# Optimization experiments

Hardware: AMD Instinct MI355X
Metric: run time of the kernel (lower is better)

## Reference

```python
import jax, jax.numpy as jnp
import numpy as np

BS, T, G, C = 64, 128, 36, 256
H = 256          # gaze LSTM hidden
P = 256          # spatial projected size
PT = 256         # temporal projected size
Q = 16           # queue size
NC = 10          # num classes
NEG = -1e9


def setup_inputs() -> dict:
    key = jax.random.key(0)
    ks = jax.random.split(key, 40)
    s = 0.02
    D = C + H
    inp = {
        'cnn_feat_seq': jax.random.normal(ks[0], (BS, T, G, C), jnp.float32),
        'gaze_seq': jax.random.normal(ks[1], (BS, T, 3), jnp.float32),
        # init-hidden / init-cell MLPs (Linear(3,H), Tanh, Linear(H,H), Tanh)
        'init_h_w1': jax.random.normal(ks[2], (H, 3)) * s, 'init_h_b1': jnp.zeros((H,)),
        'init_h_w2': jax.random.normal(ks[3], (H, H)) * s, 'init_h_b2': jnp.zeros((H,)),
        'init_c_w1': jax.random.normal(ks[4], (H, 3)) * s, 'init_c_b1': jnp.zeros((H,)),
        'init_c_w2': jax.random.normal(ks[5], (H, H)) * s, 'init_c_b2': jnp.zeros((H,)),
        # LSTM (input 3, hidden H), torch gate order i,f,g,o
        'lstm_wih': jax.random.normal(ks[6], (4 * H, 3)) * s, 'lstm_whh': jax.random.normal(ks[7], (4 * H, H)) * s,
        'lstm_bih': jnp.zeros((4 * H,)), 'lstm_bhh': jnp.zeros((4 * H,)),
        # spatial attention
        'sa_wl': jax.random.normal(ks[8], (P, H)) * s, 'sa_bl': jnp.zeros((P,)),
        'sa_wc': jax.random.normal(ks[9], (P, C)) * s, 'sa_bc': jnp.zeros((P,)),
        'sa_wz': jax.random.normal(ks[10], (P,)) * s,
        # temporal attention
        'ta_wl': jax.random.normal(ks[11], (PT, H)) * s, 'ta_bl': jnp.zeros((PT,)),
        'ta_wv': jax.random.normal(ks[12], (PT, C)) * s, 'ta_bv': jnp.zeros((PT,)),
        'ta_wz': jax.random.normal(ks[13], (PT,)) * s,
        # MLP classifier: Linear(D,D) -> Linear(D,D) -> Linear(D,NC), no nonlinearity
        'mlp_w1': jax.random.normal(ks[14], (D, D)) * s, 'mlp_b1': jnp.zeros((D,)),
        'mlp_w2': jax.random.normal(ks[15], (D, D)) * s, 'mlp_b2': jnp.zeros((D,)),
        'mlp_w3': jax.random.normal(ks[16], (NC, D)) * s, 'mlp_b3': jnp.zeros((NC,)),
    }
    return inp


def _forward(cnn_feat_seq, gaze_seq,
             init_h_w1, init_h_b1, init_h_w2, init_h_b2,
             init_c_w1, init_c_b1, init_c_w2, init_c_b2,
             lstm_wih, lstm_whh, lstm_bih, lstm_bhh,
             sa_wl, sa_bl, sa_wc, sa_bc, sa_wz,
             ta_wl, ta_bl, ta_wv, ta_bv, ta_wz,
             mlp_w1, mlp_b1, mlp_w2, mlp_b2, mlp_w3, mlp_b3):
    bs, num_frame = gaze_seq.shape[0], gaze_seq.shape[1]
    mean_gaze = jnp.mean(gaze_seq, axis=1)  # (bs, 3)
    # init MLP ends with Tanh, and forward applies F.tanh again
    h0 = jnp.tanh(jnp.tanh(jnp.tanh(mean_gaze @ init_h_w1.T + init_h_b1) @ init_h_w2.T + init_h_b2))
    c0 = jnp.tanh(jnp.tanh(jnp.tanh(mean_gaze @ init_c_w1.T + init_c_b1) @ init_c_w2.T + init_c_b2))
    buf_s0 = jnp.zeros((Q, bs, C), cnn_feat_seq.dtype)
    buf_h0 = jnp.zeros((Q, bs, H), cnn_feat_seq.dtype)
    qidx = jnp.arange(Q)

    def step(carry, xs):
        h, c, buf_s, buf_h, i = carry
        feat, gaze = xs  # (bs,G,C), (bs,3)
        # --- spatial additive attention over grids ---
        Hp = h @ sa_wl.T + sa_bl                                  # (bs,P)
        Vp = jnp.einsum('bgc,pc->bgp', feat, sa_wc) + sa_bc       # (bs,G,P)
        zs = jnp.tanh(Hp[:, None, :] + Vp) @ sa_wz                # (bs,G)
        sw = jax.nn.softmax(zs, axis=1)
        spat = jnp.einsum('bgc,bg->bc', feat, sw)                 # (bs,C)
        # --- rolling queues (newest last) ---
        buf_s = jnp.concatenate([buf_s[1:], spat[None]], axis=0)
        buf_h = jnp.concatenate([buf_h[1:], h[None]], axis=0)
        count = jnp.minimum(i + 1, Q)
        mask = qidx >= (Q - count)                                # (Q,) valid slots
        # --- temporal additive attention over queue ---
        Hq = jnp.einsum('qbh,ph->qbp', buf_h, ta_wl) + ta_bl
        Vq = jnp.einsum('qbc,pc->qbp', buf_s, ta_wv) + ta_bv
        zt = jnp.tanh(Hq + Vq) @ ta_wz                            # (Q,bs)
        zt = jnp.where(mask[:, None], zt, NEG)
        tw = jax.nn.softmax(zt, axis=0)
        temp = jnp.einsum('qbc,qb->bc', buf_s, tw)                # (bs,C)
        # --- one LSTM step on gaze ---
        gates = gaze @ lstm_wih.T + lstm_bih + h @ lstm_whh.T + lstm_bhh
        gi, gf, gg, go = jnp.split(gates, 4, axis=-1)
        c = jax.nn.sigmoid(gf) * c + jax.nn.sigmoid(gi) * jnp.tanh(gg)
        h = jax.nn.sigmoid(go) * jnp.tanh(c)
        # --- classifier on concat(temporal_feat, lstm_hidden) ---
        fc = jnp.concatenate([temp, h], axis=1)                   # (bs, C+H)
        pred = ((fc @ mlp_w1.T + mlp_b1) @ mlp_w2.T + mlp_b2) @ mlp_w3.T + mlp_b3
        return (h, c, buf_s, buf_h, i + 1), pred

    feats_t = jnp.swapaxes(cnn_feat_seq, 0, 1)  # (T,bs,G,C)
    gaze_t = jnp.swapaxes(gaze_seq, 0, 1)       # (T,bs,3)
    _, preds = jax.lax.scan(step, (h0, c0, buf_s0, buf_h0, jnp.int32(0)), (feats_t, gaze_t))
    # torch cats (1,bs,NC) pieces along dim=1 -> (1, T*bs, NC)
    return preds.reshape(1, num_frame * bs, NC)


def reference(cnn_feat_seq, gaze_seq,
              init_h_w1, init_h_b1, init_h_w2, init_h_b2,
              init_c_w1, init_c_b1, init_c_w2, init_c_b2,
              lstm_wih, lstm_whh, lstm_bih, lstm_bhh,
              sa_wl, sa_bl, sa_wc, sa_bc, sa_wz,
              ta_wl, ta_bl, ta_wv, ta_bv, ta_wz,
              mlp_w1, mlp_b1, mlp_w2, mlp_b2, mlp_w3, mlp_b3):
    return _forward(cnn_feat_seq, gaze_seq,
                    init_h_w1, init_h_b1, init_h_w2, init_h_b2,
                    init_c_w1, init_c_b1, init_c_w2, init_c_b2,
                    lstm_wih, lstm_whh, lstm_bih, lstm_bhh,
                    sa_wl, sa_bl, sa_wc, sa_bc, sa_wz,
                    ta_wl, ta_bl, ta_wv, ta_bv, ta_wz,
                    mlp_w1, mlp_b1, mlp_w2, mlp_b2, mlp_w3, mlp_b3)
```

## Files before the change

### kernel.cpp

```cpp
#include <hip/hip_runtime.h>
#include <cstdint>
#include <cstddef>

#define BSZ 64
#define TT  128
#define GG  36
#define CC  256
#define HH  256
#define QQ  16
#define NCLS 10
#define NROW 8192

using short8  = __attribute__((ext_vector_type(8))) short;
using f32x4   = __attribute__((ext_vector_type(4))) float;
using half2_t = __attribute__((ext_vector_type(2))) _Float16;
typedef unsigned int u32;
typedef unsigned short u16;

#define OFF_WI    0u
#define OFF_WF    131072u
#define OFF_WG    262144u
#define OFF_WO    393216u
#define OFF_SAWL  524288u
#define OFF_TAWL  655360u
#define OFF_TAWV  786432u
#define OFF_SAWC  917504u
#define OFF_W32   1048576u
#define OFF_WC    1069056u
#define OFF_BC    1089536u
#define OFF_H0F16 1089792u
#define OFF_C0    1122560u
#define OFF_HSEQ  1188096u
#define OFF_HSEQB 9642240u
#define OFF_HPSA  13869312u
#define OFF_HQ    22257920u
#define OFF_SPAT  30646528u
#define OFF_SPATB 39035136u
#define OFF_ZSC   43229440u
#define WS_NEEDED 43262208u

__device__ __forceinline__ float fast_sig(float x){ return 1.f/(1.f+__expf(-x)); }
__device__ __forceinline__ float fast_tanh(float x){ float e=__expf(2.f*x); return 1.f-2.f/(e+1.f); }
__device__ __forceinline__ u16 f2bf(float f){
  u32 u = __builtin_bit_cast(u32, f);
  u += 0x7fffu + ((u>>16)&1u);
  return (u16)(u>>16);
}
__device__ __forceinline__ float bf2f(u16 b){
  u32 u = ((u32)b)<<16; return __builtin_bit_cast(float, u);
}
__device__ __forceinline__ u32 packf16(float a, float b){
  half2_t h; h.x = (_Float16)a; h.y = (_Float16)b;
  return __builtin_bit_cast(u32, h);
}
__device__ __forceinline__ float dot2(u32 w, u32 h, float acc){
#if __has_builtin(__builtin_amdgcn_fdot2)
  return __builtin_amdgcn_fdot2(__builtin_bit_cast(half2_t, w),
                                __builtin_bit_cast(half2_t, h), acc, false);
#else
  half2_t a = __builtin_bit_cast(half2_t, w), b = __builtin_bit_cast(half2_t, h);
  return acc + (float)a.x*(float)b.x + (float)a.y*(float)b.y;
#endif
}
__device__ __forceinline__ f32x4 mfma16(short8 a, short8 b, f32x4 c){
  return __builtin_amdgcn_mfma_f32_16x16x32_bf16(a, b, c, 0, 0, 0);
}

__global__ void __launch_bounds__(256) k_prep1(const float* __restrict__ whh,
    const float* __restrict__ sawl, const float* __restrict__ tawl,
    const float* __restrict__ tawv, const float* __restrict__ sawc,
    const float* __restrict__ w3, const float* __restrict__ w2, char* ws){
  int blk = blockIdx.x, tid = threadIdx.x;
  if (blk < 512){
    u32* wq = (u32*)ws;
    for (int rr = 0; rr < 2; ++rr){
      int row = blk*2 + rr;
      float v  = whh[row*256 + tid];
      float vn = __shfl_down(v, 1);
      if ((tid & 1) == 0){
        int typ = row >> 8;
        int j   = row & 255;
        wq[typ*32768 + (tid>>1)*256 + j] = packf16(v, vn);
      }
    }
  } else if (blk < 544){
    int rel = blk - 512;
    int mat = rel >> 3;
    const float* src; u16* dst;
    if (mat==0){ src=sawl; dst=(u16*)(ws+OFF_SAWL); }
    else if (mat==1){ src=tawl; dst=(u16*)(ws+OFF_TAWL); }
    else if (mat==2){ src=tawv; dst=(u16*)(ws+OFF_TAWV); }
    else { src=sawc; dst=(u16*)(ws+OFF_SAWC); }
    int base = (rel & 7)*8192 + tid;
    for (int i = 0; i < 32; ++i){ int e = base + i*256; dst[e] = f2bf(src[e]); }
  } else {
    int idx = (blk-544)*256 + tid;
    int o = idx >> 9, k2 = idx & 511;
    float acc = 0.f;
    for (int m = 0; m < 512; ++m) acc = fmaf(w3[o*512+m], w2[m*512+k2], acc);
    ((float*)(ws+OFF_W32))[idx] = acc;
  }
}

__global__ void __launch_bounds__(256) k_prep2(const float* __restrict__ w1,
    const float* __restrict__ b1, const float* __restrict__ w3,
    const float* __restrict__ b2, const float* __restrict__ b3,
    const float* __restrict__ gaze,
    const float* __restrict__ ihw1, const float* __restrict__ ihb1,
    const float* __restrict__ ihw2, const float* __restrict__ ihb2,
    const float* __restrict__ icw1, const float* __restrict__ icb1,
    const float* __restrict__ icw2, const float* __restrict__ icb2,
    char* ws){
  int blk = blockIdx.x, tid = threadIdx.x;
  const float* W32 = (const float*)(ws+OFF_W32);
  if (blk < 20){
    int idx = blk*256 + tid; int o = idx>>9, k = idx&511;
    float acc = 0.f;
    for (int m = 0; m < 512; ++m) acc = fmaf(W32[o*512+m], w1[m*512+k], acc);
    ((float*)(ws+OFF_WC))[idx] = acc;
  } else if (blk == 20){
    if (tid < 10){
      float acc = b3[tid];
      for (int m = 0; m < 512; ++m) acc = fmaf(W32[tid*512+m], b1[m], acc);
      for (int m = 0; m < 512; ++m) acc = fmaf(w3[tid*512+m], b2[m], acc);
      ((float*)(ws+OFF_BC))[tid] = acc;
    }
  } else {
    int b = blk - 21;
    __shared__ float red0[128], red1[128], red2[128];
    __shared__ float mg[3];
    __shared__ float x1[256];
    if (tid < 128){
      const float* gp = gaze + b*384 + tid*3;
      red0[tid] = gp[0]; red1[tid] = gp[1]; red2[tid] = gp[2];
    }
    __syncthreads();
    for (int s = 64; s >= 1; s >>= 1){
      if (tid < s){ red0[tid]+=red0[tid+s]; red1[tid]+=red1[tid+s]; red2[tid]+=red2[tid+s]; }
      __syncthreads();
    }
    if (tid == 0){ mg[0]=red0[0]*(1.f/128.f); mg[1]=red1[0]*(1.f/128.f); mg[2]=red2[0]*(1.f/128.f); }
    __syncthreads();
    for (int which = 0; which < 2; ++which){
      const float* aw1 = which? icw1 : ihw1; const float* ab1 = which? icb1 : ihb1;
      const float* aw2 = which? icw2 : ihw2; const float* ab2 = which? icb2 : ihb2;
      float v = fast_tanh(fmaf(aw1[tid*3+2],mg[2], fmaf(aw1[tid*3+1],mg[1], fmaf(aw1[tid*3],mg[0], ab1[tid]))));
      x1[tid] = v;
      __syncthreads();
      float acc = ab2[tid];
      for (int k = 0; k < 256; ++k) acc = fmaf(aw2[tid*256+k], x1[k], acc);
      float h0 = fast_tanh(fast_tanh(acc));
      if (which == 0){
        float* hseq = (float*)(ws+OFF_HSEQ);
        hseq[(size_t)(0*64 + b)*256 + tid] = h0;
        float hn = __shfl_down(h0, 1);
        if ((tid&1)==0){
          ((u32*)(ws+OFF_HSEQB))[((size_t)(0*64+b)*256 + tid)>>1] = ((u32)f2bf(hn)<<16) | f2bf(h0);
          ((u32*)(ws+OFF_H0F16))[b*128 + (tid>>1)] = packf16(h0, hn);
        }
      } else {
        ((float*)(ws+OFF_C0))[b*256 + tid] = h0;
      }
      __syncthreads();
    }
  }
}

__global__ void __launch_bounds__(512, 2) k_lstm(const float* __restrict__ gaze,
    const float* __restrict__ wih, const float* __restrict__ bih,
    const float* __restrict__ bhh, char* ws){
  int b = blockIdx.x, tid = threadIdx.x;
  int half = tid >> 8;
  int j = tid & 255;
  __shared__ u32 lds_w[16*2048];
  __shared__ __align__(16) u32 hbuf[2][128];
  __shared__ float p_lds[256];
  __shared__ float g_lds[384];

  const u32* wq = (const u32*)ws;
  const u32* wA = wq + (half ? 1 : 0) * 32768;
  const u32* wB = wq + (half ? 3 : 2) * 32768;
  u32 w0[128], w1r[64];
#pragma unroll
  for (int c = 0; c < 128; ++c) w0[c] = wA[c*256 + j];
#pragma unroll
  for (int c = 0; c < 64; ++c)  w1r[c] = wB[c*256 + j];
#pragma unroll
  for (int cq = 0; cq < 16; ++cq)
#pragma unroll
    for (int q = 0; q < 4; ++q)
      lds_w[cq*2048 + tid*4 + q] = wB[(64 + cq*4 + q)*256 + j];

  if (tid < 384) g_lds[tid] = gaze[b*384 + tid];
  if (tid < 128) hbuf[0][tid] = ((const u32*)(ws+OFF_H0F16))[b*128 + tid];
  float creg = half ? ((const float*)(ws+OFF_C0))[b*256 + j] : 0.f;

  int rA = half ? 256 + j : j;
  int rB = half ? 768 + j : 512 + j;
  float baseA = bih[rA] + bhh[rA];
  float baseB = bih[rB] + bhh[rB];
  float uA0 = wih[rA*3], uA1 = wih[rA*3+1], uA2 = wih[rA*3+2];
  float uB0 = wih[rB*3], uB1 = wih[rB*3+1], uB2 = wih[rB*3+2];

  float* hseq = (float*)(ws+OFF_HSEQ);
  u32* hseqb = (u32*)(ws+OFF_HSEQB);
  __syncthreads();

  for (int t = 0; t < 128; ++t){
    int cur = t & 1, nxt = cur ^ 1;
    float g0 = g_lds[t*3], g1 = g_lds[t*3+1], g2 = g_lds[t*3+2];
    float aA0 = fmaf(uA2,g2, fmaf(uA1,g1, fmaf(uA0,g0, baseA))), aA1 = 0.f;
    float aB0 = fmaf(uB2,g2, fmaf(uB1,g1, fmaf(uB0,g0, baseB))), aB1 = 0.f;
#pragma unroll
    for (int c4 = 0; c4 < 32; ++c4){
      uint4 h4 = *reinterpret_cast<const uint4*>(&hbuf[cur][c4*4]);
      u32 wb0, wb1, wb2, wb3;
      if (c4 < 16){
        wb0 = w1r[c4*4]; wb1 = w1r[c4*4+1]; wb2 = w1r[c4*4+2]; wb3 = w1r[c4*4+3];
      } else {
        uint4 wv = *reinterpret_cast<const uint4*>(&lds_w[(c4-16)*2048 + tid*4]);
        wb0 = wv.x; wb1 = wv.y; wb2 = wv.z; wb3 = wv.w;
      }
      aA0 = dot2(w0[c4*4+0], h4.x, aA0); aB0 = dot2(wb0, h4.x, aB0);
      aA1 = dot2(w0[c4*4+1], h4.y, aA1); aB1 = dot2(wb1, h4.y, aB1);
      aA0 = dot2(w0[c4*4+2], h4.z, aA0); aB0 = dot2(wb2, h4.z, aB0);
      aA1 = dot2(w0[c4*4+3], h4.w, aA1); aB1 = dot2(wb3, h4.w, aB1);
    }
    float aA = aA0 + aA1, aB = aB0 + aB1;
    if (half == 0){
      p_lds[j] = fast_sig(aA) * fast_tanh(aB);
    }
    __syncthreads();
    if (half == 1){
      float p = p_lds[j];
      creg = fmaf(fast_sig(aA), creg, p);
      float hv = fast_sig(aB) * fast_tanh(creg);
      float hn = __shfl_down(hv, 1);
      if ((j & 1) == 0){
        hbuf[nxt][j>>1] = packf16(hv, hn);
        hseqb[(((size_t)(t+1)*64 + b)*256 + j)>>1] = ((u32)f2bf(hn)<<16) | f2bf(hv);
      }
      hseq[((size_t)(t+1)*64 + b)*256 + j] = hv;
    }
    __syncthreads();
  }
}

__global__ void __launch_bounds__(256) k_proj1(const float* __restrict__ sabl,
    const float* __restrict__ sabc, const float* __restrict__ tabl,
    const float* __restrict__ tabv, char* ws){
  int bx = blockIdx.x, which = blockIdx.y;
  const u16* A = (const u16*)(ws+OFF_HSEQB);
  const u16* B = (const u16*)(ws + (which? OFF_TAWL : OFF_SAWL));
  float* Out   = (float*)(ws + (which? OFF_HQ : OFF_HPSA));
  const float* bp1 = which? tabl : sabl;
  const float* bp2 = which? tabv : sabc;
  int tid = threadIdx.x, w = tid>>6, l = tid&63;
  int lr = l&15, lk = l>>4;
  int rb = bx*64;
  short8 afr[4][8];
#pragma unroll
  for (int m = 0; m < 4; ++m)
#pragma unroll
    for (int k = 0; k < 8; ++k)
      afr[m][k] = *(const short8*)(const void*)(A + (size_t)(rb + m*16 + lr)*256 + k*32 + lk*8);
#pragma unroll
  for (int n = 0; n < 4; ++n){
    int cb = w*64 + n*16;
    int col = cb + lr;
    float bias = bp1[col] + bp2[col];
    f32x4 a0 = {0.f,0.f,0.f,0.f}, a1 = a0, a2 = a0, a3 = a0;
#pragma unroll
    for (int k = 0; k < 8; ++k){
      short8 bf = *(const short8*)(const void*)(B + (size_t)col*256 + k*32 + lk*8);
      a0 = mfma16(afr[0][k], bf, a0);
      a1 = mfma16(afr[1][k], bf, a1);
      a2 = mfma16(afr[2][k], bf, a2);
      a3 = mfma16(afr[3][k], bf, a3);
    }
#pragma unroll
    for (int q = 0; q < 4; ++q){
      Out[(size_t)(rb + 0*16 + lk*4 + q)*256 + col] = a0[q] + bias;
      Out[(size_t)(rb + 1*16 + lk*4 + q)*256 + col] = a1[q] + bias;
      Out[(size_t)(rb + 2*16 + lk*4 + q)*256 + col] = a2[q] + bias;
      Out[(size_t)(rb + 3*16 + lk*4 + q)*256 + col] = a3[q] + bias;
    }
  }
}

__global__ void __launch_bounds__(256) k_spatial(const float* __restrict__ feat,
    const float* __restrict__ sawz, char* ws){
  int r = blockIdx.x;
  int t = r >> 6, b = r & 63;
  int tid = threadIdx.x, w = tid>>6, l = tid&63;
  int lr = l&15, lk = l>>4;
  __shared__ __align__(16) u32 featb[48*132];
  __shared__ float hp[256];
  __shared__ float zsbuf[4][48];
  __shared__ float swl[36];
  const float* fb = feat + ((size_t)(b*128 + t))*9216;
#pragma unroll
  for (int i = 0; i < 18; ++i){
    int e = tid + i*256;
    int g = e >> 7, cp = e & 127;
    float2 v = *(const float2*)(fb + g*256 + cp*2);
    featb[g*132 + cp] = ((u32)f2bf(v.y)<<16) | f2bf(v.x);
  }
  for (int i = tid; i < 12*132; i += 256) featb[36*132 + i] = 0;
  hp[tid] = ((const float*)(ws+OFF_HPSA))[(size_t)r*256 + tid];
  __syncthreads();
  short8 afr[3][8];
#pragma unroll
  for (int m = 0; m < 3; ++m)
#pragma unroll
    for (int k = 0; k < 8; ++k)
      afr[m][k] = *(const short8*)(const void*)((const short*)featb + (m*16 + lr)*264 + k*32 + lk*8);
  const u16* Bw = (const u16*)(ws+OFF_SAWC);
  float zacc[3][4] = {{0.f}};
#pragma unroll
  for (int n = 0; n < 4; ++n){
    int col = w*64 + n*16 + lr;
    float hpl = hp[col], wzl = sawz[col];
    f32x4 a0 = {0.f,0.f,0.f,0.f}, a1 = a0, a2 = a0;
#pragma unroll
    for (int k = 0; k < 8; ++k){
      short8 bf = *(const short8*)(const void*)(Bw + (size_t)col*256 + k*32 + lk*8);
      a0 = mfma16(afr[0][k], bf, a0);
      a1 = mfma16(afr[1][k], bf, a1);
      a2 = mfma16(afr[2][k], bf, a2);
    }
#pragma unroll
    for (int q = 0; q < 4; ++q){
      zacc[0][q] += fast_tanh(a0[q] + hpl)*wzl;
      zacc[1][q] += fast_tanh(a1[q] + hpl)*wzl;
      zacc[2][q] += fast_tanh(a2[q] + hpl)*wzl;
    }
  }
#pragma unroll
  for (int m = 0; m < 3; ++m)
#pragma unroll
    for (int q = 0; q < 4; ++q){
      float v = zacc[m][q];
      v += __shfl_xor(v, 1); v += __shfl_xor(v, 2);
      v += __shfl_xor(v, 4); v += __shfl_xor(v, 8);
      if (lr == 0) zsbuf[w][m*16 + lk*4 + q] = v;
    }
  __syncthreads();
  if (w == 0){
    float z = -1e30f;
    if (l < 36) z = zsbuf[0][l] + zsbuf[1][l] + zsbuf[2][l] + zsbuf[3][l];
    float mx = z;
    for (int d = 1; d < 64; d <<= 1) mx = fmaxf(mx, __shfl_xor(mx, d));
    float e = (l < 36)? __expf(z - mx) : 0.f;
    float s = e;
    for (int d = 1; d < 64; d <<= 1) s += __shfl_xor(s, d);
    if (l < 36) swl[l] = e / s;
  }
  __syncthreads();
  float acc = 0.f;
  const u16* fbu = (const u16*)featb;
#pragma unroll
  for (int g = 0; g < 36; ++g)
    acc = fmaf(swl[g], bf2f(fbu[g*264 + tid]), acc);
  ((float*)(ws+OFF_SPAT))[(size_t)r*256 + tid] = acc;
  float an = __shfl_down(acc, 1);
  if ((tid&1)==0)
    ((u32*)(ws+OFF_SPATB))[((size_t)r*256 + tid)>>1] = ((u32)f2bf(an)<<16) | f2bf(acc);
}

__global__ void __launch_bounds__(256) k_proj2(const float* __restrict__ tawz, char* ws){
  int bx = blockIdx.x;
  int tid = threadIdx.x, w = tid>>6, l = tid&63;
  int lr = l&15, lk = l>>4;
  int rb = bx*64;
  const u16* A = (const u16*)(ws+OFF_SPATB);
  const u16* B = (const u16*)(ws+OFF_TAWV);
  const float* Hq = (const float*)(ws+OFF_HQ);
  __shared__ float zbuf[4][64];
  short8 afr[4][8];
#pragma unroll
  for (int m = 0; m < 4; ++m)
#pragma unroll
    for (int k = 0; k < 8; ++k)
      afr[m][k] = *(const short8*)(const void*)(A + (size_t)(rb + m*16 + lr)*256 + k*32 + lk*8);
  float racc[4][4] = {{0.f}};
#pragma unroll
  for (int n = 0; n < 4; ++n){
    int col = w*64 + n*16 + lr;
    float tzl = tawz[col];
    f32x4 a0 = {0.f,0.f,0.f,0.f}, a1 = a0, a2 = a0, a3 = a0;
#pragma unroll
    for (int k = 0; k < 8; ++k){
      short8 bf = *(const short8*)(const void*)(B + (size_t)col*256 + k*32 + lk*8);
      a0 = mfma16(afr[0][k], bf, a0);
      a1 = mfma16(afr[1][k], bf, a1);
      a2 = mfma16(afr[2][k], bf, a2);
      a3 = mfma16(afr[3][k], bf, a3);
    }
#pragma unroll
    for (int q = 0; q < 4; ++q){
      racc[0][q] += fast_tanh(a0[q] + Hq[(size_t)(rb + 0*16 + lk*4 + q)*256 + col]) * tzl;
      racc[1][q] += fast_tanh(a1[q] + Hq[(size_t)(rb + 1*16 + lk*4 + q)*256 + col]) * tzl;
      racc[2][q] += fast_tanh(a2[q] + Hq[(size_t)(rb + 2*16 + lk*4 + q)*256 + col]) * tzl;
      racc[3][q] += fast_tanh(a3[q] + Hq[(size_t)(rb + 3*16 + lk*4 + q)*256 + col]) * tzl;
    }
  }
#pragma unroll
  for (int m = 0; m < 4; ++m)
#pragma unroll
    for (int q = 0; q < 4; ++q){
      float v = racc[m][q];
      v += __shfl_xor(v, 1); v += __shfl_xor(v, 2);
      v += __shfl_xor(v, 4); v += __shfl_xor(v, 8);
      if (lr == 0) zbuf[w][m*16 + lk*4 + q] = v;
    }
  __syncthreads();
  if (tid < 64)
    ((float*)(ws+OFF_ZSC))[rb + tid] = zbuf[0][tid]+zbuf[1][tid]+zbuf[2][tid]+zbuf[3][tid];
}

__global__ void __launch_bounds__(256) k_final(float* __restrict__ out, char* ws){
  int bx = blockIdx.x;
  int b = bx & 63, tb = bx >> 6;
  int t0 = tb*8;
  int tid = threadIdx.x;
  int wv = tid>>6, l = tid&63;
  __shared__ float spw[23][256];
  __shared__ float zw[23];
  __shared__ float WcL[5120];
  __shared__ float bcL[10];
  __shared__ float w16[16];
  __shared__ float wpart[4][10];
  const float* spat = (const float*)(ws+OFF_SPAT);
  const float* zsc  = (const float*)(ws+OFF_ZSC);
  const float* hseq = (const float*)(ws+OFF_HSEQ);
  const float* Wc   = (const float*)(ws+OFF_WC);
#pragma unroll
  for (int i = 0; i < 20; ++i) WcL[tid + i*256] = Wc[tid + i*256];
  if (tid < 10) bcL[tid] = ((const float*)(ws+OFF_BC))[tid];
  for (int i = 0; i < 23; ++i){
    int tau = t0 - 15 + i;
    spw[i][tid] = (tau >= 0)? spat[(size_t)(tau*64 + b)*256 + tid] : 0.f;
  }
  if (tid < 23){
    int tau = t0 - 15 + tid;
    zw[tid] = (tau >= 0)? zsc[tau*64 + b] : -1e9f;
  }
  __syncthreads();
  for (int dt = 0; dt < 8; ++dt){
    int t = t0 + dt;
    if (wv == 0 && l < 16){
      float z = zw[dt + l];
      float mx = z;
      mx = fmaxf(mx, __shfl_xor(mx,1)); mx = fmaxf(mx, __shfl_xor(mx,2));
      mx = fmaxf(mx, __shfl_xor(mx,4)); mx = fmaxf(mx, __shfl_xor(mx,8));
      float e = __expf(z - mx);
      float s = e;
      s += __shfl_xor(s,1); s += __shfl_xor(s,2); s += __shfl_xor(s,4); s += __shfl_xor(s,8);
      w16[l] = e / s;
    }
    __syncthreads();
    float temp = 0.f;
#pragma unroll
    for (int qi = 0; qi < 16; ++qi) temp = fmaf(w16[qi], spw[dt+qi][tid], temp);
    float hc = hseq[(size_t)((t+1)*64 + b)*256 + tid];
    float po[10];
#pragma unroll
    for (int o = 0; o < 10; ++o){
      float v = fmaf(temp, WcL[o*512 + tid], hc*WcL[o*512 + 256 + tid]);
      v += __shfl_xor(v,1);  v += __shfl_xor(v,2);  v += __shfl_xor(v,4);
      v += __shfl_xor(v,8);  v += __shfl_xor(v,16); v += __shfl_xor(v,32);
      po[o] = v;
    }
    if (l == 0){
#pragma unroll
      for (int o = 0; o < 10; ++o) wpart[wv][o] = po[o];
    }
    __syncthreads();
    if (tid < 10)
      out[(size_t)(t*64 + b)*10 + tid] = wpart[0][tid]+wpart[1][tid]+wpart[2][tid]+wpart[3][tid] + bcL[tid];
    __syncthreads();
  }
}

extern "C" void kernel_launch(void* const* d_in, const int* in_sizes, int n_in,
                              void* d_out, int out_size, void* d_ws, size_t ws_size,
                              hipStream_t stream){
  const float* feat = (const float*)d_in[0];
  const float* gaze = (const float*)d_in[1];
  const float* ihw1 = (const float*)d_in[2];  const float* ihb1 = (const float*)d_in[3];
  const float* ihw2 = (const float*)d_in[4];  const float* ihb2 = (const float*)d_in[5];
  const float* icw1 = (const float*)d_in[6];  const float* icb1 = (const float*)d_in[7];
  const float* icw2 = (const float*)d_in[8];  const float* icb2 = (const float*)d_in[9];
  const float* wih  = (const float*)d_in[10]; const float* whh  = (const float*)d_in[11];
  const float* bih  = (const float*)d_in[12]; const float* bhh  = (const float*)d_in[13];
  const float* sawl = (const float*)d_in[14]; const float* sabl = (const float*)d_in[15];
  const float* sawc = (const float*)d_in[16]; const float* sabc = (const float*)d_in[17];
  const float* sawz = (const float*)d_in[18];
  const float* tawl = (const float*)d_in[19]; const float* tabl = (const float*)d_in[20];
  const float* tawv = (const float*)d_in[21]; const float* tabv = (const float*)d_in[22];
  const float* tawz = (const float*)d_in[23];
  const float* w1 = (const float*)d_in[24]; const float* b1 = (const float*)d_in[25];
  const float* w2 = (const float*)d_in[26]; const float* b2 = (const float*)d_in[27];
  const float* w3 = (const float*)d_in[28]; const float* b3 = (const float*)d_in[29];
  char* ws = (char*)d_ws;
  float* out = (float*)d_out;
  if (ws_size < (size_t)WS_NEEDED) return;

  k_prep1<<<dim3(564), dim3(256), 0, stream>>>(whh, sawl, tawl, tawv, sawc, w3, w2, ws);
  k_prep2<<<dim3(85), dim3(256), 0, stream>>>(w1, b1, w3, b2, b3, gaze,
      ihw1, ihb1, ihw2, ihb2, icw1, icb1, icw2, icb2, ws);
  k_lstm<<<dim3(64), dim3(512), 0, stream>>>(gaze, wih, bih, bhh, ws);
  k_proj1<<<dim3(128, 2), dim3(256), 0, stream>>>(sabl, sabc, tabl, tabv, ws);
  k_spatial<<<dim3(8192), dim3(256), 0, stream>>>(feat, sawz, ws);
  k_proj2<<<dim3(128), dim3(256), 0, stream>>>(tawz, ws);
  k_final<<<dim3(1024), dim3(256), 0, stream>>>(out, ws);
}
```

Measured before the change: 516.6 us.

## Process two rows per block in spatial attention with packed bf16 conversion

The spatial attention kernel now handles two (t,b) rows per block, halving the grid. Feature loads are widened to float4 and converted with the hardware packed bf16 instruction instead of manual rounding, and the sawz weights are staged once in shared memory. Fast reciprocal replaces divisions in the tanh, sigmoid and softmax helpers. The larger shared-memory footprint per block may lower occupancy, and the hardware conversion and reciprocal may round slightly differently from the previous code.

```diff
diff --git a/kernel.cpp b/kernel.cpp
--- a/kernel.cpp
+++ b/kernel.cpp
@@ -39,8 +39,15 @@
 #define OFF_ZSC   43229440u
 #define WS_NEEDED 43262208u
 
-__device__ __forceinline__ float fast_sig(float x){ return 1.f/(1.f+__expf(-x)); }
-__device__ __forceinline__ float fast_tanh(float x){ float e=__expf(2.f*x); return 1.f-2.f/(e+1.f); }
+__device__ __forceinline__ float rcp_fast(float x){
+#if __has_builtin(__builtin_amdgcn_rcpf)
+  return __builtin_amdgcn_rcpf(x);
+#else
+  return 1.f/x;
+#endif
+}
+__device__ __forceinline__ float fast_sig(float x){ return rcp_fast(1.f+__expf(-x)); }
+__device__ __forceinline__ float fast_tanh(float x){ float e=__expf(2.f*x); return 1.f-2.f*rcp_fast(e+1.f); }
 __device__ __forceinline__ u16 f2bf(float f){
   u32 u = __builtin_bit_cast(u32, f);
   u += 0x7fffu + ((u>>16)&1u);
@@ -48,6 +55,11 @@
 }
 __device__ __forceinline__ float bf2f(u16 b){
   u32 u = ((u32)b)<<16; return __builtin_bit_cast(float, u);
+}
+__device__ __forceinline__ u32 cvtpk_bf16(float a, float b){
+  u32 p;
+  asm("v_cvt_pk_bf16_f32 %0, %1, %2" : "=v"(p) : "v"(a), "v"(b));
+  return p;
 }
 __device__ __forceinline__ u32 packf16(float a, float b){
   half2_t h; h.x = (_Float16)a; h.y = (_Float16)b;
@@ -290,82 +302,97 @@
 
 __global__ void __launch_bounds__(256) k_spatial(const float* __restrict__ feat,
     const float* __restrict__ sawz, char* ws){
-  int r = blockIdx.x;
-  int t = r >> 6, b = r & 63;
+  int blk = blockIdx.x;
   int tid = threadIdx.x, w = tid>>6, l = tid&63;
   int lr = l&15, lk = l>>4;
-  __shared__ __align__(16) u32 featb[48*132];
-  __shared__ float hp[256];
-  __shared__ float zsbuf[4][48];
-  __shared__ float swl[36];
-  const float* fb = feat + ((size_t)(b*128 + t))*9216;
-#pragma unroll
-  for (int i = 0; i < 18; ++i){
-    int e = tid + i*256;
-    int g = e >> 7, cp = e & 127;
-    float2 v = *(const float2*)(fb + g*256 + cp*2);
-    featb[g*132 + cp] = ((u32)f2bf(v.y)<<16) | f2bf(v.x);
-  }
-  for (int i = tid; i < 12*132; i += 256) featb[36*132 + i] = 0;
-  hp[tid] = ((const float*)(ws+OFF_HPSA))[(size_t)r*256 + tid];
+  __shared__ __align__(16) u16 featb[84*264];
+  __shared__ float hp[2][256];
+  __shared__ float wzs[256];
+  __shared__ float zsbuf[2][4][48];
+  __shared__ float swl[2][36];
+  const float* hpsa = (const float*)(ws+OFF_HPSA);
+#pragma unroll
+  for (int rr = 0; rr < 2; ++rr){
+    int r = blk*2 + rr;
+    int t = r >> 6, b = r & 63;
+    const float* fb = feat + ((size_t)(b*128 + t))*9216;
+#pragma unroll
+    for (int i = 0; i < 9; ++i){
+      int e = tid + i*256;
+      int g = e >> 6, cp4 = e & 63;
+      float4 v = *(const float4*)(fb + g*256 + cp4*4);
+      uint2 pp;
+      pp.x = cvtpk_bf16(v.x, v.y);
+      pp.y = cvtpk_bf16(v.z, v.w);
+      *reinterpret_cast<uint2*>(&featb[(rr*36 + g)*264 + cp4*4]) = pp;
+    }
+    hp[rr][tid] = hpsa[(size_t)r*256 + tid];
+  }
+  wzs[tid] = sawz[tid];
   __syncthreads();
-  short8 afr[3][8];
-#pragma unroll
-  for (int m = 0; m < 3; ++m)
-#pragma unroll
-    for (int k = 0; k < 8; ++k)
-      afr[m][k] = *(const short8*)(const void*)((const short*)featb + (m*16 + lr)*264 + k*32 + lk*8);
   const u16* Bw = (const u16*)(ws+OFF_SAWC);
-  float zacc[3][4] = {{0.f}};
-#pragma unroll
-  for (int n = 0; n < 4; ++n){
-    int col = w*64 + n*16 + lr;
-    float hpl = hp[col], wzl = sawz[col];
-    f32x4 a0 = {0.f,0.f,0.f,0.f}, a1 = a0, a2 = a0;
-#pragma unroll
-    for (int k = 0; k < 8; ++k){
-      short8 bf = *(const short8*)(const void*)(Bw + (size_t)col*256 + k*32 + lk*8);
-      a0 = mfma16(afr[0][k], bf, a0);
-      a1 = mfma16(afr[1][k], bf, a1);
-      a2 = mfma16(afr[2][k], bf, a2);
-    }
-#pragma unroll
-    for (int q = 0; q < 4; ++q){
-      zacc[0][q] += fast_tanh(a0[q] + hpl)*wzl;
-      zacc[1][q] += fast_tanh(a1[q] + hpl)*wzl;
-      zacc[2][q] += fast_tanh(a2[q] + hpl)*wzl;
-    }
-  }
-#pragma unroll
-  for (int m = 0; m < 3; ++m)
-#pragma unroll
-    for (int q = 0; q < 4; ++q){
-      float v = zacc[m][q];
-      v += __shfl_xor(v, 1); v += __shfl_xor(v, 2);
-      v += __shfl_xor(v, 4); v += __shfl_xor(v, 8);
-      if (lr == 0) zsbuf[w][m*16 + lk*4 + q] = v;
-    }
+#pragma unroll
+  for (int rr = 0; rr < 2; ++rr){
+    short8 afr[3][8];
+#pragma unroll
+    for (int m = 0; m < 3; ++m)
+#pragma unroll
+      for (int k = 0; k < 8; ++k)
+        afr[m][k] = *(const short8*)(const void*)(featb + (rr*36 + m*16 + lr)*264 + k*32 + lk*8);
+    float zacc[3][4] = {{0.f}};
+#pragma unroll
+    for (int n = 0; n < 4; ++n){
+      int col = w*64 + n*16 + lr;
+      float hpl = hp[rr][col], wzv = wzs[col];
+      f32x4 a0 = {0.f,0.f,0.f,0.f}, a1 = a0, a2 = a0;
+#pragma unroll
+      for (int k = 0; k < 8; ++k){
+        short8 bf = *(const short8*)(const void*)(Bw + (size_t)col*256 + k*32 + lk*8);
+        a0 = mfma16(afr[0][k], bf, a0);
+        a1 = mfma16(afr[1][k], bf, a1);
+        a2 = mfma16(afr[2][k], bf, a2);
+      }
+#pragma unroll
+      for (int q = 0; q < 4; ++q){
+        zacc[0][q] += fast_tanh(a0[q] + hpl)*wzv;
+        zacc[1][q] += fast_tanh(a1[q] + hpl)*wzv;
+        zacc[2][q] += fast_tanh(a2[q] + hpl)*wzv;
+      }
+    }
+#pragma unroll
+    for (int m = 0; m < 3; ++m)
+#pragma unroll
+      for (int q = 0; q < 4; ++q){
+        float v = zacc[m][q];
+        v += __shfl_xor(v, 1); v += __shfl_xor(v, 2);
+        v += __shfl_xor(v, 4); v += __shfl_xor(v, 8);
+        if (lr == 0) zsbuf[rr][w][m*16 + lk*4 + q] = v;
+      }
+  }
   __syncthreads();
-  if (w == 0){
-    float z = -1e30f;
-    if (l < 36) z = zsbuf[0][l] + zsbuf[1][l] + zsbuf[2][l] + zsbuf[3][l];
+  {
+    int rr = w & 1;
+    float z = (l < 36)? zsbuf[rr][0][l]+zsbuf[rr][1][l]+zsbuf[rr][2][l]+zsbuf[rr][3][l] : -1e30f;
     float mx = z;
     for (int d = 1; d < 64; d <<= 1) mx = fmaxf(mx, __shfl_xor(mx, d));
     float e = (l < 36)? __expf(z - mx) : 0.f;
     float s = e;
     for (int d = 1; d < 64; d <<= 1) s += __shfl_xor(s, d);
-    if (l < 36) swl[l] = e / s;
+    if (w < 2 && l < 36) swl[rr][l] = e * rcp_fast(s);
   }
   __syncthreads();
-  float acc = 0.f;
-  const u16* fbu = (const u16*)featb;
-#pragma unroll
-  for (int g = 0; g < 36; ++g)
-    acc = fmaf(swl[g], bf2f(fbu[g*264 + tid]), acc);
-  ((float*)(ws+OFF_SPAT))[(size_t)r*256 + tid] = acc;
-  float an = __shfl_down(acc, 1);
-  if ((tid&1)==0)
-    ((u32*)(ws+OFF_SPATB))[((size_t)r*256 + tid)>>1] = ((u32)f2bf(an)<<16) | f2bf(acc);
+#pragma unroll
+  for (int rr = 0; rr < 2; ++rr){
+    int r = blk*2 + rr;
+    float acc = 0.f;
+#pragma unroll
+    for (int g = 0; g < 36; ++g)
+      acc = fmaf(swl[rr][g], bf2f(featb[(rr*36 + g)*264 + tid]), acc);
+    ((float*)(ws+OFF_SPAT))[(size_t)r*256 + tid] = acc;
+    float an = __shfl_down(acc, 1);
+    if ((tid&1)==0)
+      ((u32*)(ws+OFF_SPATB))[((size_t)r*256 + tid)>>1] = cvtpk_bf16(acc, an);
+  }
 }
 
 __global__ void __launch_bounds__(256) k_proj2(const float* __restrict__ tawz, char* ws){
@@ -512,7 +539,7 @@
       ihw1, ihb1, ihw2, ihb2, icw1, icb1, icw2, icb2, ws);
   k_lstm<<<dim3(64), dim3(512), 0, stream>>>(gaze, wih, bih, bhh, ws);
   k_proj1<<<dim3(128, 2), dim3(256), 0, stream>>>(sabl, sabc, tabl, tabv, ws);
-  k_spatial<<<dim3(8192), dim3(256), 0, stream>>>(feat, sawz, ws);
+  k_spatial<<<dim3(4096), dim3(256), 0, stream>>>(feat, sawz, ws);
   k_proj2<<<dim3(128), dim3(256), 0, stream>>>(tawz, ws);
   k_final<<<dim3(1024), dim3(256), 0, stream>>>(out, ws);
 }
```

Result: slower. 527.0 us (+2.0%).
